# Performance work log

Measured on AMD Instinct MI355X. Metric: run time of the kernel, lower is better.

## Reference

```python
import jax, jax.numpy as jnp
import numpy as np

N = 50000   # nodes
E = 800000  # edges
F = 128     # feat_dim
I = 128     # internal_dim
G = 64      # graphs in batch
EPS = 1e-5


def setup_inputs() -> dict:
    key = jax.random.key(0)
    ks = jax.random.split(key, 32)
    s = 0.1
    inp = {
        'x': jax.random.normal(ks[0], (N, F), dtype=jnp.float32),
        'edge_index': jax.random.randint(ks[1], (2, E), 0, N, dtype=jnp.int64),
        'batch': jnp.sort(jax.random.randint(ks[2], (N,), 0, G, dtype=jnp.int64)),
        # InitialSubnet: Linear(F->I) + BN(I)
        'init_W': jax.random.normal(ks[3], (F, I)) * s,
        'init_b': jnp.zeros((I,)),
        'init_g': jnp.ones((I,)),
        'init_bt': jnp.zeros((I,)),
        # 2 middle EdgeConv subnets: Linear(2I->I) + BN(I)
        'mid_W': jax.random.normal(ks[4], (2, 2 * I, I)) * s,
        'mid_b': jnp.zeros((2, I)),
        'mid_g': jnp.ones((2, I)),
        'mid_bt': jnp.zeros((2, I)),
        # 1 er / 1 pr receptor-specific EdgeConv subnet each
        'er_W': jax.random.normal(ks[5], (1, 2 * I, I)) * s,
        'er_b': jnp.zeros((1, I)),
        'er_g': jnp.ones((1, I)),
        'er_bt': jnp.zeros((1, I)),
        'pr_W': jax.random.normal(ks[6], (1, 2 * I, I)) * s,
        'pr_b': jnp.zeros((1, I)),
        'pr_g': jnp.ones((1, I)),
        'pr_bt': jnp.zeros((1, I)),
        # 3 shared posts: Linear(I->2) + BN(2)
        'spost_W': jax.random.normal(ks[7], (3, I, 2)) * s,
        'spost_b': jnp.zeros((3, 2)),
        'spost_g': jnp.ones((3, 2)),
        'spost_bt': jnp.zeros((3, 2)),
        # 1 er post / 1 pr post: Linear(I->1) + BN(1)
        'erpost_W': jax.random.normal(ks[8], (1, I, 1)) * s,
        'erpost_b': jnp.zeros((1, 1)),
        'erpost_g': jnp.ones((1, 1)),
        'erpost_bt': jnp.zeros((1, 1)),
        'prpost_W': jax.random.normal(ks[9], (1, I, 1)) * s,
        'prpost_b': jnp.zeros((1, 1)),
        'prpost_g': jnp.ones((1, 1)),
        'prpost_bt': jnp.zeros((1, 1)),
    }
    return inp


def _bn(h, g, b):
    # BatchNorm1d in training mode: batch stats over the row dim, biased var
    m = jnp.mean(h, axis=0)
    v = jnp.var(h, axis=0)
    return (h - m) * jax.lax.rsqrt(v + EPS) * g + b


def _edgeconv(h, src, dst, W, b, g, bt):
    # PyG EdgeConv: msg = nn(cat([x_i, x_j - x_i])), aggr=max over incoming edges
    x_i = h[dst]                      # [E, I]
    x_j = h[src]                      # [E, I]
    msg = jnp.concatenate([x_i, x_j - x_i], axis=-1) @ W + b  # [E, I]
    msg = jax.nn.elu(_bn(msg, g, bt))
    out = jax.ops.segment_max(msg, dst, num_segments=N)
    return jnp.where(jnp.isneginf(out), 0.0, out)  # isolated nodes -> 0


def _post(h, batch, counts, W, b, g, bt):
    # elu(BN(Linear(h))) then global_mean_pool; dropout is identity (eval)
    h2 = jax.nn.elu(_bn(h @ W + b, g, bt))
    pooled = jax.ops.segment_sum(h2, batch, num_segments=G)
    return pooled / counts[:, None]


def reference(x, edge_index, batch,
              init_W, init_b, init_g, init_bt,
              mid_W, mid_b, mid_g, mid_bt,
              er_W, er_b, er_g, er_bt,
              pr_W, pr_b, pr_g, pr_bt,
              spost_W, spost_b, spost_g, spost_bt,
              erpost_W, erpost_b, erpost_g, erpost_bt,
              prpost_W, prpost_b, prpost_g, prpost_bt):
    src, dst = edge_index[0], edge_index[1]
    counts = jnp.maximum(jax.ops.segment_sum(jnp.ones((N,), x.dtype), batch, num_segments=G), 1.0)

    outs = []
    # InitialSubnet: gelu(BN(Linear(x)))
    h = jax.nn.gelu(_bn(x @ init_W + init_b, init_g, init_bt), approximate=False)
    outs.append(_post(h, batch, counts, spost_W[0], spost_b[0], spost_g[0], spost_bt[0]))

    for l in range(2):
        h = _edgeconv(h, src, dst, mid_W[l], mid_b[l], mid_g[l], mid_bt[l])
        outs.append(_post(h, batch, counts, spost_W[l + 1], spost_b[l + 1], spost_g[l + 1], spost_bt[l + 1]))

    er_h = h
    pr_h = h
    for l in range(1):
        er_h = _edgeconv(er_h, src, dst, er_W[l], er_b[l], er_g[l], er_bt[l])
        er_out = _post(er_h, batch, counts, erpost_W[l], erpost_b[l], erpost_g[l], erpost_bt[l])
        pr_h = _edgeconv(pr_h, src, dst, pr_W[l], pr_b[l], pr_g[l], pr_bt[l])
        pr_out = _post(pr_h, batch, counts, prpost_W[l], prpost_b[l], prpost_g[l], prpost_bt[l])
        outs.append(jnp.concatenate([er_out, pr_out], axis=-1))

    agg = outs[0]
    for o in outs[1:]:
        agg = agg + o
    return agg  # [G, 2]
```

## Files before the change

kernel.cpp:

```cpp
#include <hip/hip_runtime.h>
#include <math.h>

#define EPS 1e-5f

typedef float f32x4v __attribute__((ext_vector_type(4)));
typedef short s16x8  __attribute__((ext_vector_type(8)));

__device__ __forceinline__ float elu_f(float x) { return x > 0.f ? x : expm1f(x); }
__device__ __forceinline__ float blo(unsigned u) { return __uint_as_float(u << 16); }
__device__ __forceinline__ float bhi(unsigned u) { return __uint_as_float(u & 0xffff0000u); }
__device__ __forceinline__ unsigned f2b(float f) {
  unsigned u = __float_as_uint(f);
  unsigned r = ((u >> 16) & 1u) + 0x7fffu;
  return (u + r) >> 16;
}
__device__ __forceinline__ unsigned pack2(float a, float b) {
  return f2b(a) | (f2b(b) << 16);
}

__global__ __launch_bounds__(256) void prep_all(const float* __restrict__ init_W,
    const float* __restrict__ mid_W, const float* __restrict__ er_W,
    const float* __restrict__ pr_W, const float* __restrict__ mid_g,
    const float* __restrict__ er_g, const float* __restrict__ pr_g,
    unsigned short* __restrict__ WT) {
  int grp = blockIdx.x >> 6;
  int i = (blockIdx.x & 63) * 256 + threadIdx.x;
  if (i >= 16384) return;
  int k = i >> 7, c = i & 127;
  if (grp == 0) {
    WT[c * 128 + k] = (unsigned short)f2b(init_W[k * 128 + c]);
    return;
  }
  const float* W; const float* g; unsigned short* Wd; unsigned short* W2;
  if (grp == 1)      { W = mid_W;             g = mid_g;       Wd = WT + 1 * 16384; W2 = WT + 2 * 16384; }
  else if (grp == 2) { W = mid_W + 256 * 128; g = mid_g + 128; Wd = WT + 3 * 16384; W2 = WT + 4 * 16384; }
  else if (grp == 3) { W = er_W;              g = er_g;        Wd = WT + 5 * 16384; W2 = WT + 6 * 16384; }
  else               { W = pr_W;              g = pr_g;        Wd = WT + 7 * 16384; W2 = WT + 8 * 16384; }
  float sg = (g[c] >= 0.f) ? 1.f : -1.f;
  float w1 = W[k * 128 + c];
  float w2 = W[(k + 128) * 128 + c];
  Wd[c * 128 + k] = (unsigned short)f2b((w1 - w2) * sg);
  W2[c * 128 + k] = (unsigned short)f2b(w2 * sg);
}

template<int XF32, int NMAT, int STATS>
__global__ __launch_bounds__(256, 3) void gemm_mfma(const void* __restrict__ Xv,
    const unsigned short* __restrict__ W0t, const unsigned short* __restrict__ W1t,
    const unsigned short* __restrict__ W2t, const unsigned short* __restrict__ W3t,
    unsigned short* __restrict__ Y0, unsigned short* __restrict__ Y1,
    unsigned short* __restrict__ Y2, unsigned short* __restrict__ Y3,
    float* __restrict__ stOut, int Nrows) {
  int tid = threadIdx.x, lane = tid & 63, wv = tid >> 6;
  int r0 = blockIdx.x * 64;
  int rlo = lane & 15, kg = lane >> 4;
  s16x8 zf = {0, 0, 0, 0, 0, 0, 0, 0};
  s16x8 af[4][4];
#pragma unroll
  for (int rg = 0; rg < 4; ++rg) {
    int arow = r0 + rg * 16 + rlo;
    if (arow < Nrows) {
      if (XF32) {
        const float* xr = (const float*)Xv + (size_t)arow * 128 + kg * 8;
#pragma unroll
        for (int s2 = 0; s2 < 4; ++s2) {
          float4 a = *(const float4*)(xr + s2 * 32);
          float4 b = *(const float4*)(xr + s2 * 32 + 4);
          s16x8 t;
          t[0] = (short)f2b(a.x); t[1] = (short)f2b(a.y);
          t[2] = (short)f2b(a.z); t[3] = (short)f2b(a.w);
          t[4] = (short)f2b(b.x); t[5] = (short)f2b(b.y);
          t[6] = (short)f2b(b.z); t[7] = (short)f2b(b.w);
          af[rg][s2] = t;
        }
      } else {
        const unsigned short* xr = (const unsigned short*)Xv + (size_t)arow * 128 + kg * 8;
#pragma unroll
        for (int s2 = 0; s2 < 4; ++s2) af[rg][s2] = *(const s16x8*)(xr + s2 * 32);
      }
    } else {
#pragma unroll
      for (int s2 = 0; s2 < 4; ++s2) af[rg][s2] = zf;
    }
  }
  const unsigned short* Ws[4] = {W0t, W1t, W2t, W3t};
  unsigned short* Ys[4] = {Y0, Y1, Y2, Y3};
#pragma unroll
  for (int o = 0; o < NMAT; ++o) {
    const unsigned short* Wt = Ws[o];
    unsigned short* Y = Ys[o];
#pragma unroll
    for (int t = 0; t < 2; ++t) {
      int nt = wv * 2 + t;
      const unsigned short* wp = Wt + (size_t)(nt * 16 + rlo) * 128 + kg * 8;
      s16x8 wf[4];
#pragma unroll
      for (int s2 = 0; s2 < 4; ++s2) wf[s2] = *(const s16x8*)(wp + s2 * 32);
      f32x4v acc[4];
#pragma unroll
      for (int rg = 0; rg < 4; ++rg) acc[rg] = (f32x4v){0.f, 0.f, 0.f, 0.f};
#pragma unroll
      for (int s2 = 0; s2 < 4; ++s2)
#pragma unroll
        for (int rg = 0; rg < 4; ++rg)
          acc[rg] = __builtin_amdgcn_mfma_f32_16x16x32_bf16(wf[s2], af[rg][s2], acc[rg], 0, 0, 0);
      float ps0 = 0.f, ps1 = 0.f, ps2 = 0.f, ps3 = 0.f;
      float pq0 = 0.f, pq1 = 0.f, pq2 = 0.f, pq3 = 0.f;
#pragma unroll
      for (int rg = 0; rg < 4; ++rg) {
        int arow = r0 + rg * 16 + rlo;
        if (arow < Nrows) {
          uint2 ov;
          ov.x = pack2(acc[rg][0], acc[rg][1]);
          ov.y = pack2(acc[rg][2], acc[rg][3]);
          *(uint2*)(Y + (size_t)arow * 128 + nt * 16 + kg * 4) = ov;
          if (STATS) {
            float y0 = blo(ov.x), y1 = bhi(ov.x), y2 = blo(ov.y), y3 = bhi(ov.y);
            ps0 += y0; pq0 += y0 * y0;
            ps1 += y1; pq1 += y1 * y1;
            ps2 += y2; pq2 += y2 * y2;
            ps3 += y3; pq3 += y3 * y3;
          }
        }
      }
      if (STATS) {
#pragma unroll
        for (int off = 1; off < 16; off <<= 1) {
          ps0 += __shfl_xor(ps0, off); pq0 += __shfl_xor(pq0, off);
          ps1 += __shfl_xor(ps1, off); pq1 += __shfl_xor(pq1, off);
          ps2 += __shfl_xor(ps2, off); pq2 += __shfl_xor(pq2, off);
          ps3 += __shfl_xor(ps3, off); pq3 += __shfl_xor(pq3, off);
        }
        if (rlo == 0) {
          int col = nt * 16 + kg * 4;
          float* sb = stOut + (size_t)(blockIdx.x & 15) * 256;
          atomicAdd(&sb[2 * col + 0], ps0); atomicAdd(&sb[2 * col + 1], pq0);
          atomicAdd(&sb[2 * (col + 1)], ps1); atomicAdd(&sb[2 * (col + 1) + 1], pq1);
          atomicAdd(&sb[2 * (col + 2)], ps2); atomicAdd(&sb[2 * (col + 2) + 1], pq2);
          atomicAdd(&sb[2 * (col + 3)], ps3); atomicAdd(&sb[2 * (col + 3) + 1], pq3);
        }
      }
    }
  }
}

__global__ __launch_bounds__(256) void csr_p0_count_hist(const int* __restrict__ dst,
    int* __restrict__ partials, int Ecnt,
    const int* __restrict__ batch, float* __restrict__ counts, int Nn) {
  if (blockIdx.x < 64) {
    __shared__ int cnt[256];
    cnt[threadIdx.x] = 0;
    __syncthreads();
    int i0 = blockIdx.x * 256 + threadIdx.x, stride = 64 * 256;
    for (int e = i0; e < Ecnt; e += stride) atomicAdd(&cnt[(unsigned)dst[e] >> 8], 1);
    __syncthreads();
    partials[blockIdx.x * 256 + threadIdx.x] = cnt[threadIdx.x];
  } else {
    __shared__ float lc[64];
    if (threadIdx.x < 64) lc[threadIdx.x] = 0.f;
    __syncthreads();
    int i0 = (blockIdx.x - 64) * 256 + threadIdx.x, stride = 64 * 256;
    for (int n = i0; n < Nn; n += stride) atomicAdd(&lc[batch[n]], 1.f);
    __syncthreads();
    if (threadIdx.x < 64 && lc[threadIdx.x] != 0.f)
      atomicAdd(&counts[threadIdx.x * 16], lc[threadIdx.x]);
  }
}

__global__ __launch_bounds__(256) void csr_p0_scan(const int* __restrict__ partials,
    int nblk, int* __restrict__ bucket_base, int* __restrict__ gcursor) {
  __shared__ int sc[256];
  int b = threadIdx.x;
  int s = 0;
  for (int k = 0; k < nblk; ++k) s += partials[k * 256 + b];
  sc[b] = s;
  __syncthreads();
  for (int off = 1; off < 256; off <<= 1) {
    int t = (b >= off) ? sc[b - off] : 0;
    __syncthreads();
    sc[b] += t;
    __syncthreads();
  }
  int excl = sc[b] - s;
  bucket_base[b] = excl;
  gcursor[b * 16] = excl;
  if (b == 255) bucket_base[256] = sc[255];
}

#define P1_CHUNK 4096
__global__ __launch_bounds__(256) void csr_p1_bin(const int* __restrict__ src,
    const int* __restrict__ dst, int* __restrict__ gcursor,
    unsigned* __restrict__ binned, int Ecnt) {
  __shared__ unsigned stage[P1_CHUNK];
  __shared__ int cnt[256], lbase[256], gbase[256], lcur[256], sc[256];
  int tid = threadIdx.x;
  int e0 = blockIdx.x * P1_CHUNK;
  int ecnt = Ecnt - e0; if (ecnt > P1_CHUNK) ecnt = P1_CHUNK;
  cnt[tid] = 0;
  __syncthreads();
  for (int i = tid; i < ecnt; i += 256) atomicAdd(&cnt[(unsigned)dst[e0 + i] >> 8], 1);
  __syncthreads();
  sc[tid] = cnt[tid];
  __syncthreads();
  for (int off = 1; off < 256; off <<= 1) {
    int t = (tid >= off) ? sc[tid - off] : 0;
    __syncthreads();
    sc[tid] += t;
    __syncthreads();
  }
  lbase[tid] = sc[tid] - cnt[tid];
  lcur[tid] = lbase[tid];
  gbase[tid] = (cnt[tid] > 0) ? atomicAdd(&gcursor[tid * 16], cnt[tid]) : 0;
  __syncthreads();
  for (int i = tid; i < ecnt; i += 256) {
    int d = dst[e0 + i], s = src[e0 + i];
    int bk = (unsigned)d >> 8;
    int p = atomicAdd(&lcur[bk], 1);
    stage[p] = ((unsigned)bk << 24) | ((unsigned)(d & 255) << 16) | (unsigned)s;
  }
  __syncthreads();
  for (int i = tid; i < ecnt; i += 256) {
    unsigned v = stage[i];
    int bk = v >> 24;
    binned[gbase[bk] + (i - lbase[bk])] = v;
  }
}

#define P2_CAP 12288
__global__ __launch_bounds__(256) void csr_p2_sort(const unsigned* __restrict__ binned,
    const int* __restrict__ bucket_base, unsigned short* __restrict__ csr_src,
    int* __restrict__ deg, int* __restrict__ rowstart, int Nn) {
  __shared__ unsigned short stage[P2_CAP];
  __shared__ int cnt[256], lbase[256], lcur[256], sc[256];
  int b = blockIdx.x, tid = threadIdx.x;
  int base = bucket_base[b];
  int bcnt = bucket_base[b + 1] - base;
  if (bcnt > P2_CAP) bcnt = P2_CAP;
  cnt[tid] = 0;
  __syncthreads();
  for (int i = tid; i < bcnt; i += 256) atomicAdd(&cnt[(binned[base + i] >> 16) & 255], 1);
  __syncthreads();
  sc[tid] = cnt[tid];
  __syncthreads();
  for (int off = 1; off < 256; off <<= 1) {
    int t = (tid >= off) ? sc[tid - off] : 0;
    __syncthreads();
    sc[tid] += t;
    __syncthreads();
  }
  lbase[tid] = sc[tid] - cnt[tid];
  lcur[tid] = lbase[tid];
  int node = b * 256 + tid;
  if (node < Nn) { deg[node] = cnt[tid]; rowstart[node] = base + lbase[tid]; }
  __syncthreads();
  for (int i = tid; i < bcnt; i += 256) {
    unsigned v = binned[base + i];
    int j = (v >> 16) & 255;
    int p = atomicAdd(&lcur[j], 1);
    stage[p] = (unsigned short)(v & 0xffffu);
  }
  __syncthreads();
  for (int i = tid; i < bcnt; i += 256) csr_src[base + i] = stage[i];
}

__global__ __launch_bounds__(256, 8) void conv_pass(const unsigned short* __restrict__ A,
    const unsigned short* __restrict__ B, const unsigned short* __restrict__ csr_src,
    const int* __restrict__ rowstart, const int* __restrict__ deg,
    const float* __restrict__ g, unsigned short* __restrict__ Mx,
    float* __restrict__ st, int Nn) {
  __shared__ float s_sum[128], s_ssq[128];
  int tid = threadIdx.x;
  if (tid < 128) { s_sum[tid] = 0.f; s_ssq[tid] = 0.f; }
  __syncthreads();
  int lane = tid & 63;
  int wave = __builtin_amdgcn_readfirstlane((blockIdx.x << 2) + (tid >> 6));
  int wstride = gridDim.x << 2;
  int c0 = lane * 2;
  float sg0 = (g[c0] >= 0.f) ? 1.f : -1.f;
  float sg1 = (g[c0 + 1] >= 0.f) ? 1.f : -1.f;
  const unsigned* A32 = (const unsigned*)A;
  const unsigned* B32 = (const unsigned*)B;
  unsigned* M32 = (unsigned*)Mx;
  float s0 = 0.f, ss0 = 0.f, s1 = 0.f, ss1 = 0.f;
  for (int n = wave; n < Nn; n += wstride) {
    int dg = deg[n];
    if (dg == 0) continue;
    int beg = rowstart[n];
    unsigned ua = A32[(size_t)n * 64 + lane];
    float a0 = blo(ua), a1 = bhi(ua);
    float mx0 = -INFINITY, mx1 = -INFINITY;
    int e = beg, eend = beg + dg;
    for (; e + 8 <= eend; e += 8) {
      int idx[8];
#pragma unroll
      for (int q = 0; q < 8; ++q) idx[q] = csr_src[e + q];
      unsigned uu[8];
#pragma unroll
      for (int q = 0; q < 8; ++q) uu[q] = B32[(size_t)idx[q] * 64 + lane];
#pragma unroll
      for (int q = 0; q < 8; ++q) {
        float m0 = a0 + blo(uu[q]), m1 = a1 + bhi(uu[q]);
        s0 += m0; ss0 += m0 * m0;
        s1 += m1; ss1 += m1 * m1;
        mx0 = fmaxf(mx0, m0);
        mx1 = fmaxf(mx1, m1);
      }
    }
    for (; e + 2 <= eend; e += 2) {
      int ia = csr_src[e], ib = csr_src[e + 1];
      unsigned u0 = B32[(size_t)ia * 64 + lane];
      unsigned u1 = B32[(size_t)ib * 64 + lane];
      float m00 = a0 + blo(u0), m01 = a1 + bhi(u0);
      float m10 = a0 + blo(u1), m11 = a1 + bhi(u1);
      s0 += m00 + m10; ss0 += m00 * m00 + m10 * m10;
      s1 += m01 + m11; ss1 += m01 * m01 + m11 * m11;
      mx0 = fmaxf(mx0, fmaxf(m00, m10));
      mx1 = fmaxf(mx1, fmaxf(m01, m11));
    }
    if (e < eend) {
      unsigned u0 = B32[(size_t)csr_src[e] * 64 + lane];
      float m00 = a0 + blo(u0), m01 = a1 + bhi(u0);
      s0 += m00; ss0 += m00 * m00;
      s1 += m01; ss1 += m01 * m01;
      mx0 = fmaxf(mx0, m00);
      mx1 = fmaxf(mx1, m01);
    }
    M32[(size_t)n * 64 + lane] = pack2(mx0, mx1);
  }
  atomicAdd(&s_sum[c0], s0 * sg0); atomicAdd(&s_ssq[c0], ss0);
  atomicAdd(&s_sum[c0 + 1], s1 * sg1); atomicAdd(&s_ssq[c0 + 1], ss1);
  __syncthreads();
  if (tid < 128) {
    float* sb = st + (size_t)(blockIdx.x & 15) * 256;
    atomicAdd(&sb[2 * tid], s_sum[tid]);
    atomicAdd(&sb[2 * tid + 1], s_ssq[tid]);
  }
}

__global__ __launch_bounds__(256, 8) void conv_pass_dual(
    const unsigned short* __restrict__ Aer, const unsigned short* __restrict__ Ber,
    const unsigned short* __restrict__ Apr, const unsigned short* __restrict__ Bpr,
    const unsigned short* __restrict__ csr_src,
    const int* __restrict__ rowstart, const int* __restrict__ deg,
    const float* __restrict__ g_er, const float* __restrict__ g_pr,
    unsigned short* __restrict__ Mer, unsigned short* __restrict__ Mpr,
    float* __restrict__ st_er, float* __restrict__ st_pr, int Nn) {
  __shared__ float s_e[256], s_p[256];
  int tid = threadIdx.x;
  s_e[tid] = 0.f; s_p[tid] = 0.f;
  __syncthreads();
  int lane = tid & 63;
  int wave = __builtin_amdgcn_readfirstlane((blockIdx.x << 2) + (tid >> 6));
  int wstride = gridDim.x << 2;
  int c0 = lane * 2;
  float sge0 = (g_er[c0] >= 0.f) ? 1.f : -1.f;
  float sge1 = (g_er[c0 + 1] >= 0.f) ? 1.f : -1.f;
  float sgp0 = (g_pr[c0] >= 0.f) ? 1.f : -1.f;
  float sgp1 = (g_pr[c0 + 1] >= 0.f) ? 1.f : -1.f;
  const unsigned* Ae32 = (const unsigned*)Aer;
  const unsigned* Be32 = (const unsigned*)Ber;
  const unsigned* Ap32 = (const unsigned*)Apr;
  const unsigned* Bp32 = (const unsigned*)Bpr;
  unsigned* Me32 = (unsigned*)Mer;
  unsigned* Mp32 = (unsigned*)Mpr;
  float se0 = 0.f, sse0 = 0.f, se1 = 0.f, sse1 = 0.f;
  float sp0 = 0.f, ssp0 = 0.f, sp1 = 0.f, ssp1 = 0.f;
  for (int n = wave; n < Nn; n += wstride) {
    int dg = deg[n];
    if (dg == 0) continue;
    int beg = rowstart[n];
    unsigned uae = Ae32[(size_t)n * 64 + lane];
    unsigned uap = Ap32[(size_t)n * 64 + lane];
    float ae0 = blo(uae), ae1 = bhi(uae);
    float ap0 = blo(uap), ap1 = bhi(uap);
    float mxe0 = -INFINITY, mxe1 = -INFINITY, mxp0 = -INFINITY, mxp1 = -INFINITY;
    int e = beg, eend = beg + dg;
    for (; e + 8 <= eend; e += 8) {
      int idx[8];
#pragma unroll
      for (int q = 0; q < 8; ++q) idx[q] = csr_src[e + q];
      unsigned ue[8], up[8];
#pragma unroll
      for (int q = 0; q < 8; ++q) ue[q] = Be32[(size_t)idx[q] * 64 + lane];
#pragma unroll
      for (int q = 0; q < 8; ++q) up[q] = Bp32[(size_t)idx[q] * 64 + lane];
#pragma unroll
      for (int q = 0; q < 8; ++q) {
        float me0 = ae0 + blo(ue[q]), me1 = ae1 + bhi(ue[q]);
        float mp0 = ap0 + blo(up[q]), mp1 = ap1 + bhi(up[q]);
        se0 += me0; sse0 += me0 * me0; se1 += me1; sse1 += me1 * me1;
        sp0 += mp0; ssp0 += mp0 * mp0; sp1 += mp1; ssp1 += mp1 * mp1;
        mxe0 = fmaxf(mxe0, me0); mxe1 = fmaxf(mxe1, me1);
        mxp0 = fmaxf(mxp0, mp0); mxp1 = fmaxf(mxp1, mp1);
      }
    }
    for (; e + 2 <= eend; e += 2) {
      int i0 = csr_src[e], i1 = csr_src[e + 1];
      unsigned ue0 = Be32[(size_t)i0 * 64 + lane];
      unsigned up0 = Bp32[(size_t)i0 * 64 + lane];
      unsigned ue1 = Be32[(size_t)i1 * 64 + lane];
      unsigned up1 = Bp32[(size_t)i1 * 64 + lane];
      float me0 = ae0 + blo(ue0), me1 = ae1 + bhi(ue0);
      float mp0 = ap0 + blo(up0), mp1 = ap1 + bhi(up0);
      float ne0 = ae0 + blo(ue1), ne1 = ae1 + bhi(ue1);
      float np0 = ap0 + blo(up1), np1 = ap1 + bhi(up1);
      se0 += me0 + ne0; sse0 += me0 * me0 + ne0 * ne0;
      se1 += me1 + ne1; sse1 += me1 * me1 + ne1 * ne1;
      sp0 += mp0 + np0; ssp0 += mp0 * mp0 + np0 * np0;
      sp1 += mp1 + np1; ssp1 += mp1 * mp1 + np1 * np1;
      mxe0 = fmaxf(mxe0, fmaxf(me0, ne0)); mxe1 = fmaxf(mxe1, fmaxf(me1, ne1));
      mxp0 = fmaxf(mxp0, fmaxf(mp0, np0)); mxp1 = fmaxf(mxp1, fmaxf(mp1, np1));
    }
    if (e < eend) {
      int i0 = csr_src[e];
      unsigned ue = Be32[(size_t)i0 * 64 + lane];
      unsigned up = Bp32[(size_t)i0 * 64 + lane];
      float me0 = ae0 + blo(ue), me1 = ae1 + bhi(ue);
      float mp0 = ap0 + blo(up), mp1 = ap1 + bhi(up);
      se0 += me0; sse0 += me0 * me0; se1 += me1; sse1 += me1 * me1;
      sp0 += mp0; ssp0 += mp0 * mp0; sp1 += mp1; ssp1 += mp1 * mp1;
      mxe0 = fmaxf(mxe0, me0); mxe1 = fmaxf(mxe1, me1);
      mxp0 = fmaxf(mxp0, mp0); mxp1 = fmaxf(mxp1, mp1);
    }
    Me32[(size_t)n * 64 + lane] = pack2(mxe0, mxe1);
    Mp32[(size_t)n * 64 + lane] = pack2(mxp0, mxp1);
  }
  atomicAdd(&s_e[2 * c0], se0 * sge0);       atomicAdd(&s_e[2 * c0 + 1], sse0);
  atomicAdd(&s_e[2 * (c0 + 1)], se1 * sge1); atomicAdd(&s_e[2 * (c0 + 1) + 1], sse1);
  atomicAdd(&s_p[2 * c0], sp0 * sgp0);       atomicAdd(&s_p[2 * c0 + 1], ssp0);
  atomicAdd(&s_p[2 * (c0 + 1)], sp1 * sgp1); atomicAdd(&s_p[2 * (c0 + 1) + 1], ssp1);
  __syncthreads();
  {
    float* se = st_er + (size_t)(blockIdx.x & 15) * 256;
    float* sp = st_pr + (size_t)(blockIdx.x & 15) * 256;
    atomicAdd(&se[tid], s_e[tid]);
    atomicAdd(&sp[tid], s_p[tid]);
  }
}

template<int MODE>
__global__ __launch_bounds__(256) void fused_post16(const unsigned short* __restrict__ Zb,
    const int* __restrict__ deg, const float* __restrict__ stn,
    const float* __restrict__ g, const float* __restrict__ bt,
    const float* __restrict__ Wp, unsigned short* __restrict__ Hb,
    float* __restrict__ zP, float* __restrict__ stp, int Nn, float invCnt, int P) {
  __shared__ float lscale[128], lshift[128];
  __shared__ float red[4][4];
  int tid = threadIdx.x;
  if (tid < 128) {
    float sm = 0.f, sq = 0.f;
#pragma unroll
    for (int k = 0; k < 16; ++k) {
      sm += stn[k * 256 + 2 * tid];
      sq += stn[k * 256 + 2 * tid + 1];
    }
    float mean = sm * invCnt;
    float var = sq * invCnt - mean * mean;
    float sc = g[tid] * rsqrtf(var + EPS);
    float sh = bt[tid] - mean * sc;
    if (MODE == 1 && g[tid] < 0.f) sc = -sc;
    lscale[tid] = sc; lshift[tid] = sh;
  }
  __syncthreads();
  int sub = tid & 15, c0 = sub * 8;
  float sc[8], sh[8], w0[8], w1[8];
#pragma unroll
  for (int j = 0; j < 8; ++j) {
    sc[j] = lscale[c0 + j]; sh[j] = lshift[c0 + j];
    w0[j] = Wp[(c0 + j) * P];
    w1[j] = (P > 1) ? Wp[(c0 + j) * P + 1] : 0.f;
  }
  int g0 = (blockIdx.x * 256 + tid) >> 4;
  int gstride = gridDim.x * 16;
  bool leader = (sub == 0);
  float s0 = 0.f, ss0 = 0.f, s1 = 0.f, ss1 = 0.f;
  for (int n = g0; n < Nn; n += gstride) {
    float d0 = 0.f, d1 = 0.f;
    unsigned ow[4];
    bool live = (MODE == 0) || (deg[n] > 0);
    if (live) {
      uint4 v = ((const uint4*)(Zb + (size_t)n * 128))[sub];
      unsigned w[4] = {v.x, v.y, v.z, v.w};
#pragma unroll
      for (int u = 0; u < 4; ++u) {
        float t0 = blo(w[u]) * sc[2 * u] + sh[2 * u];
        float t1 = bhi(w[u]) * sc[2 * u + 1] + sh[2 * u + 1];
        float y0, y1;
        if (MODE == 0) {
          y0 = 0.5f * t0 * (1.f + erff(t0 * 0.70710678118f));
          y1 = 0.5f * t1 * (1.f + erff(t1 * 0.70710678118f));
        } else {
          y0 = elu_f(t0); y1 = elu_f(t1);
        }
        d0 += y0 * w0[2 * u] + y1 * w0[2 * u + 1];
        d1 += y0 * w1[2 * u] + y1 * w1[2 * u + 1];
        ow[u] = pack2(y0, y1);
      }
    } else {
      ow[0] = ow[1] = ow[2] = ow[3] = 0u;
    }
    if (Hb) ((uint4*)(Hb + (size_t)n * 128))[sub] = make_uint4(ow[0], ow[1], ow[2], ow[3]);
#pragma unroll
    for (int off = 1; off < 16; off <<= 1) {
      d0 += __shfl_xor(d0, off);
      d1 += __shfl_xor(d1, off);
    }
    if (leader) {
      zP[n * 2] = d0;
      if (P > 1) zP[n * 2 + 1] = d1;
      s0 += d0; ss0 += d0 * d0; s1 += d1; ss1 += d1 * d1;
    }
  }
  s0 += __shfl_xor(s0, 16);  s0 += __shfl_xor(s0, 32);
  s1 += __shfl_xor(s1, 16);  s1 += __shfl_xor(s1, 32);
  ss0 += __shfl_xor(ss0, 16); ss0 += __shfl_xor(ss0, 32);
  ss1 += __shfl_xor(ss1, 16); ss1 += __shfl_xor(ss1, 32);
  int wv = tid >> 6;
  if ((tid & 63) == 0) { red[wv][0] = s0; red[wv][1] = s1; red[wv][2] = ss0; red[wv][3] = ss1; }
  __syncthreads();
  if (tid < 4) {
    float v = red[0][tid] + red[1][tid] + red[2][tid] + red[3][tid];
    atomicAdd(&stp[tid * 64], v);
  }
}

__global__ __launch_bounds__(256) void fused_post16_dual(
    const unsigned short* __restrict__ Mer, const unsigned short* __restrict__ Mpr,
    const int* __restrict__ deg,
    const float* __restrict__ st_er, const float* __restrict__ st_pr,
    const float* __restrict__ g_er, const float* __restrict__ bt_er,
    const float* __restrict__ g_pr, const float* __restrict__ bt_pr,
    const float* __restrict__ Wer, const float* __restrict__ Wpr,
    float* __restrict__ zP, float* __restrict__ stp_er, float* __restrict__ stp_pr,
    int Nn, float invE) {
  __shared__ float sce_l[128], she_l[128], scp_l[128], shp_l[128];
  __shared__ float red[4][4];
  int tid = threadIdx.x;
  if (tid < 128) {
    float sme = 0.f, sqe = 0.f, smp = 0.f, sqp = 0.f;
#pragma unroll
    for (int k = 0; k < 16; ++k) {
      sme += st_er[k * 256 + 2 * tid];
      sqe += st_er[k * 256 + 2 * tid + 1];
      smp += st_pr[k * 256 + 2 * tid];
      sqp += st_pr[k * 256 + 2 * tid + 1];
    }
    float mean = sme * invE;
    float var = sqe * invE - mean * mean;
    float sc = g_er[tid] * rsqrtf(var + EPS);
    she_l[tid] = bt_er[tid] - mean * sc;
    sce_l[tid] = (g_er[tid] < 0.f) ? -sc : sc;
    mean = smp * invE;
    var = sqp * invE - mean * mean;
    sc = g_pr[tid] * rsqrtf(var + EPS);
    shp_l[tid] = bt_pr[tid] - mean * sc;
    scp_l[tid] = (g_pr[tid] < 0.f) ? -sc : sc;
  }
  __syncthreads();
  int sub = tid & 15, c0 = sub * 8;
  float sce[8], she[8], scp[8], shp[8], we[8], wp[8];
#pragma unroll
  for (int j = 0; j < 8; ++j) {
    sce[j] = sce_l[c0 + j]; she[j] = she_l[c0 + j];
    scp[j] = scp_l[c0 + j]; shp[j] = shp_l[c0 + j];
    we[j] = Wer[c0 + j]; wp[j] = Wpr[c0 + j];
  }
  int g0 = (blockIdx.x * 256 + tid) >> 4;
  int gstride = gridDim.x * 16;
  bool leader = (sub == 0);
  float s0 = 0.f, ss0 = 0.f, s1 = 0.f, ss1 = 0.f;
  for (int n = g0; n < Nn; n += gstride) {
    float d0 = 0.f, d1 = 0.f;
    if (deg[n] > 0) {
      uint4 ve = ((const uint4*)(Mer + (size_t)n * 128))[sub];
      uint4 vp = ((const uint4*)(Mpr + (size_t)n * 128))[sub];
      unsigned wea[4] = {ve.x, ve.y, ve.z, ve.w};
      unsigned wpa[4] = {vp.x, vp.y, vp.z, vp.w};
#pragma unroll
      for (int u = 0; u < 4; ++u) {
        float te0 = blo(wea[u]) * sce[2 * u] + she[2 * u];
        float te1 = bhi(wea[u]) * sce[2 * u + 1] + she[2 * u + 1];
        float tp0 = blo(wpa[u]) * scp[2 * u] + shp[2 * u];
        float tp1 = bhi(wpa[u]) * scp[2 * u + 1] + shp[2 * u + 1];
        d0 += elu_f(te0) * we[2 * u] + elu_f(te1) * we[2 * u + 1];
        d1 += elu_f(tp0) * wp[2 * u] + elu_f(tp1) * wp[2 * u + 1];
      }
    }
#pragma unroll
    for (int off = 1; off < 16; off <<= 1) {
      d0 += __shfl_xor(d0, off);
      d1 += __shfl_xor(d1, off);
    }
    if (leader) {
      zP[n * 2] = d0;
      zP[n * 2 + 1] = d1;
      s0 += d0; ss0 += d0 * d0; s1 += d1; ss1 += d1 * d1;
    }
  }
  s0 += __shfl_xor(s0, 16);  s0 += __shfl_xor(s0, 32);
  s1 += __shfl_xor(s1, 16);  s1 += __shfl_xor(s1, 32);
  ss0 += __shfl_xor(ss0, 16); ss0 += __shfl_xor(ss0, 32);
  ss1 += __shfl_xor(ss1, 16); ss1 += __shfl_xor(ss1, 32);
  int wv = tid >> 6;
  if ((tid & 63) == 0) { red[wv][0] = s0; red[wv][1] = s1; red[wv][2] = ss0; red[wv][3] = ss1; }
  __syncthreads();
  if (tid < 4) {
    float v = red[0][tid] + red[1][tid] + red[2][tid] + red[3][tid];
    if (tid == 0) atomicAdd(&stp_er[0], v);
    else if (tid == 1) atomicAdd(&stp_pr[0], v);
    else if (tid == 2) atomicAdd(&stp_er[128], v);
    else atomicAdd(&stp_pr[128], v);
  }
}

__global__ __launch_bounds__(256) void post_phase2(const float* __restrict__ zP,
    const int* __restrict__ batch, const float* __restrict__ counts,
    const float* __restrict__ st, const float* __restrict__ g,
    const float* __restrict__ bt, float* __restrict__ out,
    int Nrows, int P, int coloff, float invN) {
  __shared__ float lacc[128];
  if (threadIdx.x < 128) lacc[threadIdx.x] = 0.f;
  __syncthreads();
  float m0 = st[0] * invN;
  float v0 = st[128] * invN - m0 * m0;
  float scale0 = g[0] * rsqrtf(v0 + EPS);
  float shift0 = bt[0] - m0 * scale0;
  float scale1 = 0.f, shift1 = 0.f;
  if (P > 1) {
    float m1 = st[64] * invN;
    float v1 = st[192] * invN - m1 * m1;
    scale1 = g[1] * rsqrtf(v1 + EPS);
    shift1 = bt[1] - m1 * scale1;
  }
  int i0 = blockIdx.x * 256 + threadIdx.x;
  int stride = gridDim.x * 256;
  for (int n = i0; n < Nrows; n += stride) {
    int gi = batch[n];
    float y0 = elu_f(zP[n * 2] * scale0 + shift0);
    atomicAdd(&lacc[gi * 2], y0);
    if (P > 1) {
      float y1 = elu_f(zP[n * 2 + 1] * scale1 + shift1);
      atomicAdd(&lacc[gi * 2 + 1], y1);
    }
  }
  __syncthreads();
  if (threadIdx.x < 128) {
    int gi = threadIdx.x >> 1, p = threadIdx.x & 1;
    float v = lacc[threadIdx.x];
    if (p < P && v != 0.f)
      atomicAdd(&out[gi * 2 + coloff + p], v / fmaxf(counts[gi * 16], 1.f));
  }
}

__global__ __launch_bounds__(256) void post_phase2_dual(const float* __restrict__ zP,
    const int* __restrict__ batch, const float* __restrict__ counts,
    const float* __restrict__ st_er, const float* __restrict__ st_pr,
    const float* __restrict__ g_er, const float* __restrict__ bt_er,
    const float* __restrict__ g_pr, const float* __restrict__ bt_pr,
    float* __restrict__ out, int Nrows, float invN) {
  __shared__ float lacc[128];
  if (threadIdx.x < 128) lacc[threadIdx.x] = 0.f;
  __syncthreads();
  float m0 = st_er[0] * invN;
  float v0 = st_er[128] * invN - m0 * m0;
  float scale0 = g_er[0] * rsqrtf(v0 + EPS);
  float shift0 = bt_er[0] - m0 * scale0;
  float m1 = st_pr[0] * invN;
  float v1 = st_pr[128] * invN - m1 * m1;
  float scale1 = g_pr[0] * rsqrtf(v1 + EPS);
  float shift1 = bt_pr[0] - m1 * scale1;
  int i0 = blockIdx.x * 256 + threadIdx.x;
  int stride = gridDim.x * 256;
  for (int n = i0; n < Nrows; n += stride) {
    int gi = batch[n];
    float y0 = elu_f(zP[n * 2] * scale0 + shift0);
    float y1 = elu_f(zP[n * 2 + 1] * scale1 + shift1);
    atomicAdd(&lacc[gi * 2], y0);
    atomicAdd(&lacc[gi * 2 + 1], y1);
  }
  __syncthreads();
  if (threadIdx.x < 128) {
    int gi = threadIdx.x >> 1, p = threadIdx.x & 1;
    float v = lacc[threadIdx.x];
    if (v != 0.f)
      atomicAdd(&out[gi * 2 + p], v / fmaxf(counts[gi * 16], 1.f));
  }
}

extern "C" void kernel_launch(void* const* d_in, const int* in_sizes, int n_in,
                              void* d_out, int out_size, void* d_ws, size_t ws_size,
                              hipStream_t stream) {
  const float* x       = (const float*)d_in[0];
  const int*   ei      = (const int*)d_in[1];
  const int*   batch   = (const int*)d_in[2];
  const float* init_W  = (const float*)d_in[3];
  const float* init_g  = (const float*)d_in[5];
  const float* init_bt = (const float*)d_in[6];
  const float* mid_W   = (const float*)d_in[7];
  const float* mid_g   = (const float*)d_in[9];
  const float* mid_bt  = (const float*)d_in[10];
  const float* er_W    = (const float*)d_in[11];
  const float* er_g    = (const float*)d_in[13];
  const float* er_bt   = (const float*)d_in[14];
  const float* pr_W    = (const float*)d_in[15];
  const float* pr_g    = (const float*)d_in[17];
  const float* pr_bt   = (const float*)d_in[18];
  const float* spost_W  = (const float*)d_in[19];
  const float* spost_g  = (const float*)d_in[21];
  const float* spost_bt = (const float*)d_in[22];
  const float* erpost_W  = (const float*)d_in[23];
  const float* erpost_g  = (const float*)d_in[25];
  const float* erpost_bt = (const float*)d_in[26];
  const float* prpost_W  = (const float*)d_in[27];
  const float* prpost_g  = (const float*)d_in[29];
  const float* prpost_bt = (const float*)d_in[30];

  int N = in_sizes[0] / 128;
  int E = in_sizes[1] / 2;
  float invN = 1.f / (float)N;
  float invE = 1.f / (float)E;
  float* out = (float*)d_out;

  const int CONV_GRID = 2048;
  int nbuck = (N + 255) >> 8;

  size_t NB = (size_t)N * 128;
  unsigned short* Hb  = (unsigned short*)d_ws;
  unsigned short* Tb0 = Hb + NB;
  unsigned short* Tb1 = Tb0 + NB;
  unsigned short* Tb2 = Tb1 + NB;
  unsigned short* Tb3 = Tb2 + NB;
  unsigned short* MxB = Tb3 + NB;
  unsigned short* MxB2 = MxB + NB;
  float* zP     = (float*)(MxB2 + NB);
  float* counts = zP + (size_t)2 * N;
  float* stats  = counts + 1024;
  float* post   = stats + 5 * 4096;
  unsigned short* WT = (unsigned short*)(post + 5 * 512);
  int* deg        = (int*)(WT + 9 * 16384);
  int* rowstart   = deg + N;
  int* bucketbase = rowstart + N;
  int* gcursor    = bucketbase + 320;
  int* partials   = gcursor + 256 * 16;
  unsigned* binned = (unsigned*)(partials + 64 * 256);
  unsigned short* csr_src = (unsigned short*)(binned + E);

  int gemmGrid = (N + 63) / 64;

  hipMemsetAsync(d_out, 0, out_size * sizeof(float), stream);
  hipMemsetAsync(counts, 0, (1024 + 5 * 4096 + 5 * 512) * sizeof(float), stream);

  prep_all<<<320, 256, 0, stream>>>(init_W, mid_W, er_W, pr_W, mid_g, er_g, pr_g, WT);

  const int* e_src = ei;
  const int* e_dst = ei + E;
  csr_p0_count_hist<<<128, 256, 0, stream>>>(e_dst, partials, E, batch, counts, N);
  csr_p0_scan<<<1, 256, 0, stream>>>(partials, 64, bucketbase, gcursor);
  csr_p1_bin<<<(E + P1_CHUNK - 1) / P1_CHUNK, 256, 0, stream>>>(e_src, e_dst, gcursor, binned, E);
  csr_p2_sort<<<nbuck, 256, 0, stream>>>(binned, bucketbase, csr_src, deg, rowstart, N);

  gemm_mfma<1, 1, 1><<<gemmGrid, 256, 0, stream>>>((const void*)x, WT, nullptr, nullptr, nullptr,
                                                   Tb0, nullptr, nullptr, nullptr, stats, N);
  fused_post16<0><<<512, 256, 0, stream>>>(Tb0, deg, stats, init_g, init_bt, spost_W,
                                           Hb, zP, post + 0 * 512, N, invN, 2);
  post_phase2<<<32, 256, 0, stream>>>(zP, batch, counts, post + 0 * 512,
                                      spost_g, spost_bt, out, N, 2, 0, invN);

  gemm_mfma<0, 2, 0><<<gemmGrid, 256, 0, stream>>>((const void*)Hb,
      WT + 1 * 16384, WT + 2 * 16384, nullptr, nullptr, Tb0, Tb1, nullptr, nullptr, nullptr, N);
  conv_pass<<<CONV_GRID, 256, 0, stream>>>(Tb0, Tb1, csr_src, rowstart, deg, mid_g,
                                           MxB, stats + 1 * 4096, N);
  fused_post16<1><<<512, 256, 0, stream>>>(MxB, deg, stats + 1 * 4096, mid_g, mid_bt,
                                           spost_W + 256, Hb, zP, post + 1 * 512, N, invE, 2);
  post_phase2<<<32, 256, 0, stream>>>(zP, batch, counts, post + 1 * 512,
                                      spost_g + 2, spost_bt + 2, out, N, 2, 0, invN);

  gemm_mfma<0, 2, 0><<<gemmGrid, 256, 0, stream>>>((const void*)Hb,
      WT + 3 * 16384, WT + 4 * 16384, nullptr, nullptr, Tb0, Tb1, nullptr, nullptr, nullptr, N);
  conv_pass<<<CONV_GRID, 256, 0, stream>>>(Tb0, Tb1, csr_src, rowstart, deg, mid_g + 128,
                                           MxB, stats + 2 * 4096, N);
  fused_post16<1><<<512, 256, 0, stream>>>(MxB, deg, stats + 2 * 4096, mid_g + 128, mid_bt + 128,
                                           spost_W + 512, Hb, zP, post + 2 * 512, N, invE, 2);
  post_phase2<<<32, 256, 0, stream>>>(zP, batch, counts, post + 2 * 512,
                                      spost_g + 4, spost_bt + 4, out, N, 2, 0, invN);

  gemm_mfma<0, 4, 0><<<gemmGrid, 256, 0, stream>>>((const void*)Hb,
      WT + 5 * 16384, WT + 6 * 16384, WT + 7 * 16384, WT + 8 * 16384,
      Tb0, Tb1, Tb2, Tb3, nullptr, N);
  conv_pass_dual<<<CONV_GRID, 256, 0, stream>>>(Tb0, Tb1, Tb2, Tb3, csr_src, rowstart, deg,
                                                er_g, pr_g, MxB, MxB2,
                                                stats + 3 * 4096, stats + 4 * 4096, N);
  fused_post16_dual<<<512, 256, 0, stream>>>(MxB, MxB2, deg,
      stats + 3 * 4096, stats + 4 * 4096, er_g, er_bt, pr_g, pr_bt,
      erpost_W, prpost_W, zP, post + 3 * 512, post + 4 * 512, N, invE);
  post_phase2_dual<<<32, 256, 0, stream>>>(zP, batch, counts,
      post + 3 * 512, post + 4 * 512, erpost_g, erpost_bt, prpost_g, prpost_bt,
      out, N, invN);
}
```

Before: 428.8 us.

## Fuse BN+activation+post projection into GEMM prologue and post_phase2 into conv

Removes the separate fused_post16 pass by applying BatchNorm, GELU/ELU and the 2-wide post projection inside the next GEMM's A-fragment load. The GEMM also writes the zP values and their statistics, and post_phase2 work moves into extra blocks appended to the conv_pass grid. Weight prep is merged with the CSR histogram kernel to cut launches. This drops one full read/write of the N×128 activation per layer and several launches. In exchange the GEMM does more per-element math and register work, and the appended post blocks depend on ordering inside the conv kernel.

Result: slower. 518.3 us (+20.9%).

```diff
diff --git a/kernel.cpp b/kernel.cpp
--- a/kernel.cpp
+++ b/kernel.cpp
@@ -18,68 +18,262 @@
   return f2b(a) | (f2b(b) << 16);
 }
 
-__global__ __launch_bounds__(256) void prep_all(const float* __restrict__ init_W,
+__global__ __launch_bounds__(256) void prep_csr0(const float* __restrict__ init_W,
     const float* __restrict__ mid_W, const float* __restrict__ er_W,
     const float* __restrict__ pr_W, const float* __restrict__ mid_g,
     const float* __restrict__ er_g, const float* __restrict__ pr_g,
-    unsigned short* __restrict__ WT) {
-  int grp = blockIdx.x >> 6;
-  int i = (blockIdx.x & 63) * 256 + threadIdx.x;
-  if (i >= 16384) return;
-  int k = i >> 7, c = i & 127;
-  if (grp == 0) {
-    WT[c * 128 + k] = (unsigned short)f2b(init_W[k * 128 + c]);
-    return;
-  }
-  const float* W; const float* g; unsigned short* Wd; unsigned short* W2;
-  if (grp == 1)      { W = mid_W;             g = mid_g;       Wd = WT + 1 * 16384; W2 = WT + 2 * 16384; }
-  else if (grp == 2) { W = mid_W + 256 * 128; g = mid_g + 128; Wd = WT + 3 * 16384; W2 = WT + 4 * 16384; }
-  else if (grp == 3) { W = er_W;              g = er_g;        Wd = WT + 5 * 16384; W2 = WT + 6 * 16384; }
-  else               { W = pr_W;              g = pr_g;        Wd = WT + 7 * 16384; W2 = WT + 8 * 16384; }
-  float sg = (g[c] >= 0.f) ? 1.f : -1.f;
-  float w1 = W[k * 128 + c];
-  float w2 = W[(k + 128) * 128 + c];
-  Wd[c * 128 + k] = (unsigned short)f2b((w1 - w2) * sg);
-  W2[c * 128 + k] = (unsigned short)f2b(w2 * sg);
-}
-
-template<int XF32, int NMAT, int STATS>
+    unsigned short* __restrict__ WT,
+    const int* __restrict__ dst, int* __restrict__ partials, int Ecnt,
+    const int* __restrict__ batch, float* __restrict__ counts, int Nn) {
+  if (blockIdx.x < 320) {
+    int grp = blockIdx.x >> 6;
+    int i = (blockIdx.x & 63) * 256 + threadIdx.x;
+    if (i >= 16384) return;
+    int k = i >> 7, c = i & 127;
+    if (grp == 0) {
+      WT[c * 128 + k] = (unsigned short)f2b(init_W[k * 128 + c]);
+      return;
+    }
+    const float* W; const float* g; unsigned short* Wd; unsigned short* W2;
+    if (grp == 1)      { W = mid_W;             g = mid_g;       Wd = WT + 1 * 16384; W2 = WT + 2 * 16384; }
+    else if (grp == 2) { W = mid_W + 256 * 128; g = mid_g + 128; Wd = WT + 3 * 16384; W2 = WT + 4 * 16384; }
+    else if (grp == 3) { W = er_W;              g = er_g;        Wd = WT + 5 * 16384; W2 = WT + 6 * 16384; }
+    else               { W = pr_W;              g = pr_g;        Wd = WT + 7 * 16384; W2 = WT + 8 * 16384; }
+    float sg = (g[c] >= 0.f) ? 1.f : -1.f;
+    float w1 = W[k * 128 + c];
+    float w2 = W[(k + 128) * 128 + c];
+    Wd[c * 128 + k] = (unsigned short)f2b((w1 - w2) * sg);
+    W2[c * 128 + k] = (unsigned short)f2b(w2 * sg);
+  } else {
+    int b = blockIdx.x - 320;
+    if (b < 64) {
+      __shared__ int cnt[256];
+      cnt[threadIdx.x] = 0;
+      __syncthreads();
+      int i0 = b * 256 + threadIdx.x, stride = 64 * 256;
+      for (int e = i0; e < Ecnt; e += stride) atomicAdd(&cnt[(unsigned)dst[e] >> 8], 1);
+      __syncthreads();
+      partials[b * 256 + threadIdx.x] = cnt[threadIdx.x];
+    } else {
+      __shared__ float lc[64];
+      if (threadIdx.x < 64) lc[threadIdx.x] = 0.f;
+      __syncthreads();
+      int i0 = (b - 64) * 256 + threadIdx.x, stride = 64 * 256;
+      for (int n = i0; n < Nn; n += stride) atomicAdd(&lc[batch[n]], 1.f);
+      __syncthreads();
+      if (threadIdx.x < 64 && lc[threadIdx.x] != 0.f)
+        atomicAdd(&counts[threadIdx.x * 16], lc[threadIdx.x]);
+    }
+  }
+}
+
+__global__ __launch_bounds__(256) void csr_p0_scan(const int* __restrict__ partials,
+    int nblk, int* __restrict__ bucket_base, int* __restrict__ gcursor) {
+  __shared__ int sc[256];
+  int b = threadIdx.x;
+  int s = 0;
+  for (int k = 0; k < nblk; ++k) s += partials[k * 256 + b];
+  sc[b] = s;
+  __syncthreads();
+  for (int off = 1; off < 256; off <<= 1) {
+    int t = (b >= off) ? sc[b - off] : 0;
+    __syncthreads();
+    sc[b] += t;
+    __syncthreads();
+  }
+  int excl = sc[b] - s;
+  bucket_base[b] = excl;
+  gcursor[b * 16] = excl;
+  if (b == 255) bucket_base[256] = sc[255];
+}
+
+#define P1_CHUNK 4096
+__global__ __launch_bounds__(256) void csr_p1_bin(const int* __restrict__ src,
+    const int* __restrict__ dst, int* __restrict__ gcursor,
+    unsigned* __restrict__ binned, int Ecnt) {
+  __shared__ unsigned stage[P1_CHUNK];
+  __shared__ int cnt[256], lbase[256], gbase[256], lcur[256], sc[256];
+  int tid = threadIdx.x;
+  int e0 = blockIdx.x * P1_CHUNK;
+  int ecnt = Ecnt - e0; if (ecnt > P1_CHUNK) ecnt = P1_CHUNK;
+  cnt[tid] = 0;
+  __syncthreads();
+  for (int i = tid; i < ecnt; i += 256) atomicAdd(&cnt[(unsigned)dst[e0 + i] >> 8], 1);
+  __syncthreads();
+  sc[tid] = cnt[tid];
+  __syncthreads();
+  for (int off = 1; off < 256; off <<= 1) {
+    int t = (tid >= off) ? sc[tid - off] : 0;
+    __syncthreads();
+    sc[tid] += t;
+    __syncthreads();
+  }
+  lbase[tid] = sc[tid] - cnt[tid];
+  lcur[tid] = lbase[tid];
+  gbase[tid] = (cnt[tid] > 0) ? atomicAdd(&gcursor[tid * 16], cnt[tid]) : 0;
+  __syncthreads();
+  for (int i = tid; i < ecnt; i += 256) {
+    int d = dst[e0 + i], s = src[e0 + i];
+    int bk = (unsigned)d >> 8;
+    int p = atomicAdd(&lcur[bk], 1);
+    stage[p] = ((unsigned)bk << 24) | ((unsigned)(d & 255) << 16) | (unsigned)s;
+  }
+  __syncthreads();
+  for (int i = tid; i < ecnt; i += 256) {
+    unsigned v = stage[i];
+    int bk = v >> 24;
+    binned[gbase[bk] + (i - lbase[bk])] = v;
+  }
+}
+
+#define P2_CAP 12288
+__global__ __launch_bounds__(256) void csr_p2_sort(const unsigned* __restrict__ binned,
+    const int* __restrict__ bucket_base, unsigned short* __restrict__ csr_src,
+    int* __restrict__ deg, int* __restrict__ rowstart, int Nn) {
+  __shared__ unsigned short stage[P2_CAP];
+  __shared__ int cnt[256], lbase[256], lcur[256], sc[256];
+  int b = blockIdx.x, tid = threadIdx.x;
+  int base = bucket_base[b];
+  int bcnt = bucket_base[b + 1] - base;
+  if (bcnt > P2_CAP) bcnt = P2_CAP;
+  cnt[tid] = 0;
+  __syncthreads();
+  for (int i = tid; i < bcnt; i += 256) atomicAdd(&cnt[(binned[base + i] >> 16) & 255], 1);
+  __syncthreads();
+  sc[tid] = cnt[tid];
+  __syncthreads();
+  for (int off = 1; off < 256; off <<= 1) {
+    int t = (tid >= off) ? sc[tid - off] : 0;
+    __syncthreads();
+    sc[tid] += t;
+    __syncthreads();
+  }
+  lbase[tid] = sc[tid] - cnt[tid];
+  lcur[tid] = lbase[tid];
+  int node = b * 256 + tid;
+  if (node < Nn) { deg[node] = cnt[tid]; rowstart[node] = base + lbase[tid]; }
+  __syncthreads();
+  for (int i = tid; i < bcnt; i += 256) {
+    unsigned v = binned[base + i];
+    int j = (v >> 16) & 255;
+    int p = atomicAdd(&lcur[j], 1);
+    stage[p] = (unsigned short)(v & 0xffffu);
+  }
+  __syncthreads();
+  for (int i = tid; i < bcnt; i += 256) csr_src[base + i] = stage[i];
+}
+
+template<int XF32, int NMAT, int STATS, int ACT>
 __global__ __launch_bounds__(256, 3) void gemm_mfma(const void* __restrict__ Xv,
     const unsigned short* __restrict__ W0t, const unsigned short* __restrict__ W1t,
     const unsigned short* __restrict__ W2t, const unsigned short* __restrict__ W3t,
     unsigned short* __restrict__ Y0, unsigned short* __restrict__ Y1,
     unsigned short* __restrict__ Y2, unsigned short* __restrict__ Y3,
-    float* __restrict__ stOut, int Nrows) {
+    float* __restrict__ stOut,
+    const float* __restrict__ stn, const float* __restrict__ g,
+    const float* __restrict__ bt, const int* __restrict__ deg,
+    const float* __restrict__ Wp, float* __restrict__ zP, float* __restrict__ stp,
+    float invCnt, int Nrows) {
+  __shared__ float lsc[128], lsh[128], lw0[128], lw1[128];
   int tid = threadIdx.x, lane = tid & 63, wv = tid >> 6;
   int r0 = blockIdx.x * 64;
   int rlo = lane & 15, kg = lane >> 4;
+  if (ACT) {
+    if (tid < 128) {
+      float sm = 0.f, sq = 0.f;
+#pragma unroll
+      for (int k = 0; k < 16; ++k) {
+        sm += stn[k * 256 + 2 * tid];
+        sq += stn[k * 256 + 2 * tid + 1];
+      }
+      float mean = sm * invCnt;
+      float var = sq * invCnt - mean * mean;
+      float sc = g[tid] * rsqrtf(var + EPS);
+      float sh = bt[tid] - mean * sc;
+      if (ACT == 2 && g[tid] < 0.f) sc = -sc;
+      lsc[tid] = sc; lsh[tid] = sh;
+      lw0[tid] = Wp[tid * 2]; lw1[tid] = Wp[tid * 2 + 1];
+    }
+    __syncthreads();
+  }
   s16x8 zf = {0, 0, 0, 0, 0, 0, 0, 0};
   s16x8 af[4][4];
-#pragma unroll
-  for (int rg = 0; rg < 4; ++rg) {
-    int arow = r0 + rg * 16 + rlo;
-    if (arow < Nrows) {
-      if (XF32) {
-        const float* xr = (const float*)Xv + (size_t)arow * 128 + kg * 8;
-#pragma unroll
-        for (int s2 = 0; s2 < 4; ++s2) {
-          float4 a = *(const float4*)(xr + s2 * 32);
-          float4 b = *(const float4*)(xr + s2 * 32 + 4);
-          s16x8 t;
-          t[0] = (short)f2b(a.x); t[1] = (short)f2b(a.y);
-          t[2] = (short)f2b(a.z); t[3] = (short)f2b(a.w);
-          t[4] = (short)f2b(b.x); t[5] = (short)f2b(b.y);
-          t[6] = (short)f2b(b.z); t[7] = (short)f2b(b.w);
-          af[rg][s2] = t;
+  float d0 = 0.f, d1 = 0.f;
+  if (!ACT) {
+#pragma unroll
+    for (int rg = 0; rg < 4; ++rg) {
+      int arow = r0 + rg * 16 + rlo;
+      if (arow < Nrows) {
+        if (XF32) {
+          const float* xr = (const float*)Xv + (size_t)arow * 128 + kg * 8;
+#pragma unroll
+          for (int s2 = 0; s2 < 4; ++s2) {
+            float4 a = *(const float4*)(xr + s2 * 32);
+            float4 b = *(const float4*)(xr + s2 * 32 + 4);
+            s16x8 t;
+            t[0] = (short)f2b(a.x); t[1] = (short)f2b(a.y);
+            t[2] = (short)f2b(a.z); t[3] = (short)f2b(a.w);
+            t[4] = (short)f2b(b.x); t[5] = (short)f2b(b.y);
+            t[6] = (short)f2b(b.z); t[7] = (short)f2b(b.w);
+            af[rg][s2] = t;
+          }
+        } else {
+          const unsigned short* xr = (const unsigned short*)Xv + (size_t)arow * 128 + kg * 8;
+#pragma unroll
+          for (int s2 = 0; s2 < 4; ++s2) af[rg][s2] = *(const s16x8*)(xr + s2 * 32);
         }
       } else {
-        const unsigned short* xr = (const unsigned short*)Xv + (size_t)arow * 128 + kg * 8;
-#pragma unroll
-        for (int s2 = 0; s2 < 4; ++s2) af[rg][s2] = *(const s16x8*)(xr + s2 * 32);
+#pragma unroll
+        for (int s2 = 0; s2 < 4; ++s2) af[rg][s2] = zf;
       }
-    } else {
-#pragma unroll
-      for (int s2 = 0; s2 < 4; ++s2) af[rg][s2] = zf;
+    }
+  } else {
+    int degv[4];
+#pragma unroll
+    for (int rg = 0; rg < 4; ++rg) {
+      int arow = r0 + rg * 16 + rlo;
+      degv[rg] = (arow < Nrows) ? ((ACT == 2) ? deg[arow] : 1) : 0;
+    }
+#pragma unroll
+    for (int s2 = 0; s2 < 4; ++s2) {
+      int cb = kg * 8 + s2 * 32;
+      float sc[8], sh[8], w0[8], w1[8];
+#pragma unroll
+      for (int j = 0; j < 8; ++j) {
+        sc[j] = lsc[cb + j]; sh[j] = lsh[cb + j];
+        w0[j] = lw0[cb + j]; w1[j] = lw1[cb + j];
+      }
+#pragma unroll
+      for (int rg = 0; rg < 4; ++rg) {
+        if (degv[rg] > 0) {
+          int arow = r0 + rg * 16 + rlo;
+          uint4 v = *(const uint4*)((const unsigned short*)Xv + (size_t)arow * 128 + cb);
+          unsigned wds[4] = {v.x, v.y, v.z, v.w};
+          s16x8 t;
+          float dd0 = 0.f, dd1 = 0.f;
+#pragma unroll
+          for (int u = 0; u < 4; ++u) {
+            float t0 = blo(wds[u]) * sc[2 * u] + sh[2 * u];
+            float t1 = bhi(wds[u]) * sc[2 * u + 1] + sh[2 * u + 1];
+            float y0, y1;
+            if (ACT == 1) {
+              y0 = 0.5f * t0 * (1.f + erff(t0 * 0.70710678118f));
+              y1 = 0.5f * t1 * (1.f + erff(t1 * 0.70710678118f));
+            } else {
+              y0 = elu_f(t0); y1 = elu_f(t1);
+            }
+            unsigned pw = pack2(y0, y1);
+            t[2 * u] = (short)(pw & 0xffffu);
+            t[2 * u + 1] = (short)(pw >> 16);
+            dd0 += y0 * w0[2 * u] + y1 * w0[2 * u + 1];
+            dd1 += y0 * w1[2 * u] + y1 * w1[2 * u + 1];
+          }
+          af[rg][s2] = t;
+          if (rg == wv) { d0 += dd0; d1 += dd1; }
+        } else {
+          af[rg][s2] = zf;
+        }
+      }
     }
   }
   const unsigned short* Ws[4] = {W0t, W1t, W2t, W3t};
@@ -141,139 +335,75 @@
       }
     }
   }
-}
-
-__global__ __launch_bounds__(256) void csr_p0_count_hist(const int* __restrict__ dst,
-    int* __restrict__ partials, int Ecnt,
-    const int* __restrict__ batch, float* __restrict__ counts, int Nn) {
-  if (blockIdx.x < 64) {
-    __shared__ int cnt[256];
-    cnt[threadIdx.x] = 0;
-    __syncthreads();
-    int i0 = blockIdx.x * 256 + threadIdx.x, stride = 64 * 256;
-    for (int e = i0; e < Ecnt; e += stride) atomicAdd(&cnt[(unsigned)dst[e] >> 8], 1);
-    __syncthreads();
-    partials[blockIdx.x * 256 + threadIdx.x] = cnt[threadIdx.x];
-  } else {
-    __shared__ float lc[64];
-    if (threadIdx.x < 64) lc[threadIdx.x] = 0.f;
-    __syncthreads();
-    int i0 = (blockIdx.x - 64) * 256 + threadIdx.x, stride = 64 * 256;
-    for (int n = i0; n < Nn; n += stride) atomicAdd(&lc[batch[n]], 1.f);
-    __syncthreads();
-    if (threadIdx.x < 64 && lc[threadIdx.x] != 0.f)
-      atomicAdd(&counts[threadIdx.x * 16], lc[threadIdx.x]);
-  }
-}
-
-__global__ __launch_bounds__(256) void csr_p0_scan(const int* __restrict__ partials,
-    int nblk, int* __restrict__ bucket_base, int* __restrict__ gcursor) {
-  __shared__ int sc[256];
-  int b = threadIdx.x;
-  int s = 0;
-  for (int k = 0; k < nblk; ++k) s += partials[k * 256 + b];
-  sc[b] = s;
-  __syncthreads();
-  for (int off = 1; off < 256; off <<= 1) {
-    int t = (b >= off) ? sc[b - off] : 0;
-    __syncthreads();
-    sc[b] += t;
-    __syncthreads();
-  }
-  int excl = sc[b] - s;
-  bucket_base[b] = excl;
-  gcursor[b * 16] = excl;
-  if (b == 255) bucket_base[256] = sc[255];
-}
-
-#define P1_CHUNK 4096
-__global__ __launch_bounds__(256) void csr_p1_bin(const int* __restrict__ src,
-    const int* __restrict__ dst, int* __restrict__ gcursor,
-    unsigned* __restrict__ binned, int Ecnt) {
-  __shared__ unsigned stage[P1_CHUNK];
-  __shared__ int cnt[256], lbase[256], gbase[256], lcur[256], sc[256];
-  int tid = threadIdx.x;
-  int e0 = blockIdx.x * P1_CHUNK;
-  int ecnt = Ecnt - e0; if (ecnt > P1_CHUNK) ecnt = P1_CHUNK;
-  cnt[tid] = 0;
-  __syncthreads();
-  for (int i = tid; i < ecnt; i += 256) atomicAdd(&cnt[(unsigned)dst[e0 + i] >> 8], 1);
-  __syncthreads();
-  sc[tid] = cnt[tid];
-  __syncthreads();
-  for (int off = 1; off < 256; off <<= 1) {
-    int t = (tid >= off) ? sc[tid - off] : 0;
-    __syncthreads();
-    sc[tid] += t;
-    __syncthreads();
-  }
-  lbase[tid] = sc[tid] - cnt[tid];
-  lcur[tid] = lbase[tid];
-  gbase[tid] = (cnt[tid] > 0) ? atomicAdd(&gcursor[tid * 16], cnt[tid]) : 0;
-  __syncthreads();
-  for (int i = tid; i < ecnt; i += 256) {
-    int d = dst[e0 + i], s = src[e0 + i];
-    int bk = (unsigned)d >> 8;
-    int p = atomicAdd(&lcur[bk], 1);
-    stage[p] = ((unsigned)bk << 24) | ((unsigned)(d & 255) << 16) | (unsigned)s;
-  }
-  __syncthreads();
-  for (int i = tid; i < ecnt; i += 256) {
-    unsigned v = stage[i];
-    int bk = v >> 24;
-    binned[gbase[bk] + (i - lbase[bk])] = v;
-  }
-}
-
-#define P2_CAP 12288
-__global__ __launch_bounds__(256) void csr_p2_sort(const unsigned* __restrict__ binned,
-    const int* __restrict__ bucket_base, unsigned short* __restrict__ csr_src,
-    int* __restrict__ deg, int* __restrict__ rowstart, int Nn) {
-  __shared__ unsigned short stage[P2_CAP];
-  __shared__ int cnt[256], lbase[256], lcur[256], sc[256];
-  int b = blockIdx.x, tid = threadIdx.x;
-  int base = bucket_base[b];
-  int bcnt = bucket_base[b + 1] - base;
-  if (bcnt > P2_CAP) bcnt = P2_CAP;
-  cnt[tid] = 0;
-  __syncthreads();
-  for (int i = tid; i < bcnt; i += 256) atomicAdd(&cnt[(binned[base + i] >> 16) & 255], 1);
-  __syncthreads();
-  sc[tid] = cnt[tid];
-  __syncthreads();
-  for (int off = 1; off < 256; off <<= 1) {
-    int t = (tid >= off) ? sc[tid - off] : 0;
-    __syncthreads();
-    sc[tid] += t;
-    __syncthreads();
-  }
-  lbase[tid] = sc[tid] - cnt[tid];
-  lcur[tid] = lbase[tid];
-  int node = b * 256 + tid;
-  if (node < Nn) { deg[node] = cnt[tid]; rowstart[node] = base + lbase[tid]; }
-  __syncthreads();
-  for (int i = tid; i < bcnt; i += 256) {
-    unsigned v = binned[base + i];
-    int j = (v >> 16) & 255;
-    int p = atomicAdd(&lcur[j], 1);
-    stage[p] = (unsigned short)(v & 0xffffu);
-  }
-  __syncthreads();
-  for (int i = tid; i < bcnt; i += 256) csr_src[base + i] = stage[i];
+  if (ACT) {
+    d0 += __shfl_xor(d0, 16); d0 += __shfl_xor(d0, 32);
+    d1 += __shfl_xor(d1, 16); d1 += __shfl_xor(d1, 32);
+    int arow = r0 + wv * 16 + rlo;
+    bool rowok = arow < Nrows;
+    if (rowok && lane < 16) {
+      zP[(size_t)arow * 2] = d0;
+      zP[(size_t)arow * 2 + 1] = d1;
+    }
+    float sd0 = rowok ? d0 : 0.f, sd1 = rowok ? d1 : 0.f;
+    float q0 = sd0 * sd0, q1 = sd1 * sd1;
+#pragma unroll
+    for (int off = 1; off < 16; off <<= 1) {
+      sd0 += __shfl_xor(sd0, off); sd1 += __shfl_xor(sd1, off);
+      q0 += __shfl_xor(q0, off);   q1 += __shfl_xor(q1, off);
+    }
+    if (lane == 0) {
+      float* sb = stp + (size_t)(blockIdx.x & 15) * 4;
+      atomicAdd(sb + 0, sd0); atomicAdd(sb + 1, sd1);
+      atomicAdd(sb + 2, q0);  atomicAdd(sb + 3, q1);
+    }
+  }
 }
 
 __global__ __launch_bounds__(256, 8) void conv_pass(const unsigned short* __restrict__ A,
     const unsigned short* __restrict__ B, const unsigned short* __restrict__ csr_src,
     const int* __restrict__ rowstart, const int* __restrict__ deg,
     const float* __restrict__ g, unsigned short* __restrict__ Mx,
-    float* __restrict__ st, int Nn) {
+    float* __restrict__ st, int Nn, int convBlks,
+    const float* __restrict__ zPp, const int* __restrict__ batch,
+    const float* __restrict__ counts, const float* __restrict__ stpp,
+    const float* __restrict__ g2, const float* __restrict__ bt2,
+    float* __restrict__ out, float invN) {
   __shared__ float s_sum[128], s_ssq[128];
   int tid = threadIdx.x;
+  if ((int)blockIdx.x >= convBlks) {
+    __shared__ float lacc[128];
+    if (tid < 128) lacc[tid] = 0.f;
+    __syncthreads();
+    float S0 = 0.f, S1 = 0.f, Q0 = 0.f, Q1 = 0.f;
+#pragma unroll
+    for (int k = 0; k < 16; ++k) {
+      S0 += stpp[4 * k]; S1 += stpp[4 * k + 1];
+      Q0 += stpp[4 * k + 2]; Q1 += stpp[4 * k + 3];
+    }
+    float m0 = S0 * invN, v0 = Q0 * invN - m0 * m0;
+    float scale0 = g2[0] * rsqrtf(v0 + EPS), shift0 = bt2[0] - m0 * scale0;
+    float m1 = S1 * invN, v1 = Q1 * invN - m1 * m1;
+    float scale1 = g2[1] * rsqrtf(v1 + EPS), shift1 = bt2[1] - m1 * scale1;
+    int i0 = (blockIdx.x - convBlks) * 256 + tid;
+    int stride = 32 * 256;
+    for (int n = i0; n < Nn; n += stride) {
+      int gi = batch[n];
+      atomicAdd(&lacc[gi * 2], elu_f(zPp[n * 2] * scale0 + shift0));
+      atomicAdd(&lacc[gi * 2 + 1], elu_f(zPp[n * 2 + 1] * scale1 + shift1));
+    }
+    __syncthreads();
+    if (tid < 128) {
+      int gi = tid >> 1, p = tid & 1;
+      float v = lacc[tid];
+      if (v != 0.f) atomicAdd(&out[gi * 2 + p], v / fmaxf(counts[gi * 16], 1.f));
+    }
+    return;
+  }
   if (tid < 128) { s_sum[tid] = 0.f; s_ssq[tid] = 0.f; }
   __syncthreads();
   int lane = tid & 63;
   int wave = __builtin_amdgcn_readfirstlane((blockIdx.x << 2) + (tid >> 6));
-  int wstride = gridDim.x << 2;
+  int wstride = convBlks << 2;
   int c0 = lane * 2;
   float sg0 = (g[c0] >= 0.f) ? 1.f : -1.f;
   float sg1 = (g[c0 + 1] >= 0.f) ? 1.f : -1.f;
@@ -343,14 +473,47 @@
     const int* __restrict__ rowstart, const int* __restrict__ deg,
     const float* __restrict__ g_er, const float* __restrict__ g_pr,
     unsigned short* __restrict__ Mer, unsigned short* __restrict__ Mpr,
-    float* __restrict__ st_er, float* __restrict__ st_pr, int Nn) {
+    float* __restrict__ st_er, float* __restrict__ st_pr, int Nn, int convBlks,
+    const float* __restrict__ zPp, const int* __restrict__ batch,
+    const float* __restrict__ counts, const float* __restrict__ stpp,
+    const float* __restrict__ g2, const float* __restrict__ bt2,
+    float* __restrict__ out, float invN) {
   __shared__ float s_e[256], s_p[256];
   int tid = threadIdx.x;
+  if ((int)blockIdx.x >= convBlks) {
+    __shared__ float lacc[128];
+    if (tid < 128) lacc[tid] = 0.f;
+    __syncthreads();
+    float S0 = 0.f, S1 = 0.f, Q0 = 0.f, Q1 = 0.f;
+#pragma unroll
+    for (int k = 0; k < 16; ++k) {
+      S0 += stpp[4 * k]; S1 += stpp[4 * k + 1];
+      Q0 += stpp[4 * k + 2]; Q1 += stpp[4 * k + 3];
+    }
+    float m0 = S0 * invN, v0 = Q0 * invN - m0 * m0;
+    float scale0 = g2[0] * rsqrtf(v0 + EPS), shift0 = bt2[0] - m0 * scale0;
+    float m1 = S1 * invN, v1 = Q1 * invN - m1 * m1;
+    float scale1 = g2[1] * rsqrtf(v1 + EPS), shift1 = bt2[1] - m1 * scale1;
+    int i0 = (blockIdx.x - convBlks) * 256 + tid;
+    int stride = 32 * 256;
+    for (int n = i0; n < Nn; n += stride) {
+      int gi = batch[n];
+      atomicAdd(&lacc[gi * 2], elu_f(zPp[n * 2] * scale0 + shift0));
+      atomicAdd(&lacc[gi * 2 + 1], elu_f(zPp[n * 2 + 1] * scale1 + shift1));
+    }
+    __syncthreads();
+    if (tid < 128) {
+      int gi = tid >> 1, p = tid & 1;
+      float v = lacc[tid];
+      if (v != 0.f) atomicAdd(&out[gi * 2 + p], v / fmaxf(counts[gi * 16], 1.f));
+    }
+    return;
+  }
   s_e[tid] = 0.f; s_p[tid] = 0.f;
   __syncthreads();
   int lane = tid & 63;
   int wave = __builtin_amdgcn_readfirstlane((blockIdx.x << 2) + (tid >> 6));
-  int wstride = gridDim.x << 2;
+  int wstride = convBlks << 2;
   int c0 = lane * 2;
   float sge0 = (g_er[c0] >= 0.f) ? 1.f : -1.f;
   float sge1 = (g_er[c0 + 1] >= 0.f) ? 1.f : -1.f;
@@ -437,92 +600,6 @@
   }
 }
 
-template<int MODE>
-__global__ __launch_bounds__(256) void fused_post16(const unsigned short* __restrict__ Zb,
-    const int* __restrict__ deg, const float* __restrict__ stn,
-    const float* __restrict__ g, const float* __restrict__ bt,
-    const float* __restrict__ Wp, unsigned short* __restrict__ Hb,
-    float* __restrict__ zP, float* __restrict__ stp, int Nn, float invCnt, int P) {
-  __shared__ float lscale[128], lshift[128];
-  __shared__ float red[4][4];
-  int tid = threadIdx.x;
-  if (tid < 128) {
-    float sm = 0.f, sq = 0.f;
-#pragma unroll
-    for (int k = 0; k < 16; ++k) {
-      sm += stn[k * 256 + 2 * tid];
-      sq += stn[k * 256 + 2 * tid + 1];
-    }
-    float mean = sm * invCnt;
-    float var = sq * invCnt - mean * mean;
-    float sc = g[tid] * rsqrtf(var + EPS);
-    float sh = bt[tid] - mean * sc;
-    if (MODE == 1 && g[tid] < 0.f) sc = -sc;
-    lscale[tid] = sc; lshift[tid] = sh;
-  }
-  __syncthreads();
-  int sub = tid & 15, c0 = sub * 8;
-  float sc[8], sh[8], w0[8], w1[8];
-#pragma unroll
-  for (int j = 0; j < 8; ++j) {
-    sc[j] = lscale[c0 + j]; sh[j] = lshift[c0 + j];
-    w0[j] = Wp[(c0 + j) * P];
-    w1[j] = (P > 1) ? Wp[(c0 + j) * P + 1] : 0.f;
-  }
-  int g0 = (blockIdx.x * 256 + tid) >> 4;
-  int gstride = gridDim.x * 16;
-  bool leader = (sub == 0);
-  float s0 = 0.f, ss0 = 0.f, s1 = 0.f, ss1 = 0.f;
-  for (int n = g0; n < Nn; n += gstride) {
-    float d0 = 0.f, d1 = 0.f;
-    unsigned ow[4];
-    bool live = (MODE == 0) || (deg[n] > 0);
-    if (live) {
-      uint4 v = ((const uint4*)(Zb + (size_t)n * 128))[sub];
-      unsigned w[4] = {v.x, v.y, v.z, v.w};
-#pragma unroll
-      for (int u = 0; u < 4; ++u) {
-        float t0 = blo(w[u]) * sc[2 * u] + sh[2 * u];
-        float t1 = bhi(w[u]) * sc[2 * u + 1] + sh[2 * u + 1];
-        float y0, y1;
-        if (MODE == 0) {
-          y0 = 0.5f * t0 * (1.f + erff(t0 * 0.70710678118f));
-          y1 = 0.5f * t1 * (1.f + erff(t1 * 0.70710678118f));
-        } else {
-          y0 = elu_f(t0); y1 = elu_f(t1);
-        }
-        d0 += y0 * w0[2 * u] + y1 * w0[2 * u + 1];
-        d1 += y0 * w1[2 * u] + y1 * w1[2 * u + 1];
-        ow[u] = pack2(y0, y1);
-      }
-    } else {
-      ow[0] = ow[1] = ow[2] = ow[3] = 0u;
-    }
-    if (Hb) ((uint4*)(Hb + (size_t)n * 128))[sub] = make_uint4(ow[0], ow[1], ow[2], ow[3]);
-#pragma unroll
-    for (int off = 1; off < 16; off <<= 1) {
-      d0 += __shfl_xor(d0, off);
-      d1 += __shfl_xor(d1, off);
-    }
-    if (leader) {
-      zP[n * 2] = d0;
-      if (P > 1) zP[n * 2 + 1] = d1;
-      s0 += d0; ss0 += d0 * d0; s1 += d1; ss1 += d1 * d1;
-    }
-  }
-  s0 += __shfl_xor(s0, 16);  s0 += __shfl_xor(s0, 32);
-  s1 += __shfl_xor(s1, 16);  s1 += __shfl_xor(s1, 32);
-  ss0 += __shfl_xor(ss0, 16); ss0 += __shfl_xor(ss0, 32);
-  ss1 += __shfl_xor(ss1, 16); ss1 += __shfl_xor(ss1, 32);
-  int wv = tid >> 6;
-  if ((tid & 63) == 0) { red[wv][0] = s0; red[wv][1] = s1; red[wv][2] = ss0; red[wv][3] = ss1; }
-  __syncthreads();
-  if (tid < 4) {
-    float v = red[0][tid] + red[1][tid] + red[2][tid] + red[3][tid];
-    atomicAdd(&stp[tid * 64], v);
-  }
-}
-
 __global__ __launch_bounds__(256) void fused_post16_dual(
     const unsigned short* __restrict__ Mer, const unsigned short* __restrict__ Mpr,
     const int* __restrict__ deg,
@@ -609,45 +686,6 @@
     else if (tid == 1) atomicAdd(&stp_pr[0], v);
     else if (tid == 2) atomicAdd(&stp_er[128], v);
     else atomicAdd(&stp_pr[128], v);
-  }
-}
-
-__global__ __launch_bounds__(256) void post_phase2(const float* __restrict__ zP,
-    const int* __restrict__ batch, const float* __restrict__ counts,
-    const float* __restrict__ st, const float* __restrict__ g,
-    const float* __restrict__ bt, float* __restrict__ out,
-    int Nrows, int P, int coloff, float invN) {
-  __shared__ float lacc[128];
-  if (threadIdx.x < 128) lacc[threadIdx.x] = 0.f;
-  __syncthreads();
-  float m0 = st[0] * invN;
-  float v0 = st[128] * invN - m0 * m0;
-  float scale0 = g[0] * rsqrtf(v0 + EPS);
-  float shift0 = bt[0] - m0 * scale0;
-  float scale1 = 0.f, shift1 = 0.f;
-  if (P > 1) {
-    float m1 = st[64] * invN;
-    float v1 = st[192] * invN - m1 * m1;
-    scale1 = g[1] * rsqrtf(v1 + EPS);
-    shift1 = bt[1] - m1 * scale1;
-  }
-  int i0 = blockIdx.x * 256 + threadIdx.x;
-  int stride = gridDim.x * 256;
-  for (int n = i0; n < Nrows; n += stride) {
-    int gi = batch[n];
-    float y0 = elu_f(zP[n * 2] * scale0 + shift0);
-    atomicAdd(&lacc[gi * 2], y0);
-    if (P > 1) {
-      float y1 = elu_f(zP[n * 2 + 1] * scale1 + shift1);
-      atomicAdd(&lacc[gi * 2 + 1], y1);
-    }
-  }
-  __syncthreads();
-  if (threadIdx.x < 128) {
-    int gi = threadIdx.x >> 1, p = threadIdx.x & 1;
-    float v = lacc[threadIdx.x];
-    if (p < P && v != 0.f)
-      atomicAdd(&out[gi * 2 + coloff + p], v / fmaxf(counts[gi * 16], 1.f));
   }
 }
 
@@ -720,12 +758,12 @@
   float invE = 1.f / (float)E;
   float* out = (float*)d_out;
 
-  const int CONV_GRID = 2048;
+  const int CONV_BLKS = 2048;
   int nbuck = (N + 255) >> 8;
 
   size_t NB = (size_t)N * 128;
-  unsigned short* Hb  = (unsigned short*)d_ws;
-  unsigned short* Tb0 = Hb + NB;
+  unsigned short* TbI = (unsigned short*)d_ws;
+  unsigned short* Tb0 = TbI + NB;
   unsigned short* Tb1 = Tb0 + NB;
   unsigned short* Tb2 = Tb1 + NB;
   unsigned short* Tb3 = Tb2 + NB;
@@ -734,8 +772,9 @@
   float* zP     = (float*)(MxB2 + NB);
   float* counts = zP + (size_t)2 * N;
   float* stats  = counts + 1024;
-  float* post   = stats + 5 * 4096;
-  unsigned short* WT = (unsigned short*)(post + 5 * 512);
+  float* stp    = stats + 5 * 4096;
+  float* dpost  = stp + 3 * 64;
+  unsigned short* WT = (unsigned short*)(dpost + 2 * 512);
   int* deg        = (int*)(WT + 9 * 16384);
   int* rowstart   = deg + N;
   int* bucketbase = rowstart + N;
@@ -747,52 +786,50 @@
   int gemmGrid = (N + 63) / 64;
 
   hipMemsetAsync(d_out, 0, out_size * sizeof(float), stream);
-  hipMemsetAsync(counts, 0, (1024 + 5 * 4096 + 5 * 512) * sizeof(float), stream);
-
-  prep_all<<<320, 256, 0, stream>>>(init_W, mid_W, er_W, pr_W, mid_g, er_g, pr_g, WT);
+  hipMemsetAsync(counts, 0, (1024 + 5 * 4096 + 3 * 64 + 2 * 512) * sizeof(float), stream);
 
   const int* e_src = ei;
   const int* e_dst = ei + E;
-  csr_p0_count_hist<<<128, 256, 0, stream>>>(e_dst, partials, E, batch, counts, N);
+  prep_csr0<<<448, 256, 0, stream>>>(init_W, mid_W, er_W, pr_W, mid_g, er_g, pr_g, WT,
+                                     e_dst, partials, E, batch, counts, N);
   csr_p0_scan<<<1, 256, 0, stream>>>(partials, 64, bucketbase, gcursor);
   csr_p1_bin<<<(E + P1_CHUNK - 1) / P1_CHUNK, 256, 0, stream>>>(e_src, e_dst, gcursor, binned, E);
   csr_p2_sort<<<nbuck, 256, 0, stream>>>(binned, bucketbase, csr_src, deg, rowstart, N);
 
-  gemm_mfma<1, 1, 1><<<gemmGrid, 256, 0, stream>>>((const void*)x, WT, nullptr, nullptr, nullptr,
-                                                   Tb0, nullptr, nullptr, nullptr, stats, N);
-  fused_post16<0><<<512, 256, 0, stream>>>(Tb0, deg, stats, init_g, init_bt, spost_W,
-                                           Hb, zP, post + 0 * 512, N, invN, 2);
-  post_phase2<<<32, 256, 0, stream>>>(zP, batch, counts, post + 0 * 512,
-                                      spost_g, spost_bt, out, N, 2, 0, invN);
-
-  gemm_mfma<0, 2, 0><<<gemmGrid, 256, 0, stream>>>((const void*)Hb,
-      WT + 1 * 16384, WT + 2 * 16384, nullptr, nullptr, Tb0, Tb1, nullptr, nullptr, nullptr, N);
-  conv_pass<<<CONV_GRID, 256, 0, stream>>>(Tb0, Tb1, csr_src, rowstart, deg, mid_g,
-                                           MxB, stats + 1 * 4096, N);
-  fused_post16<1><<<512, 256, 0, stream>>>(MxB, deg, stats + 1 * 4096, mid_g, mid_bt,
-                                           spost_W + 256, Hb, zP, post + 1 * 512, N, invE, 2);
-  post_phase2<<<32, 256, 0, stream>>>(zP, batch, counts, post + 1 * 512,
-                                      spost_g + 2, spost_bt + 2, out, N, 2, 0, invN);
-
-  gemm_mfma<0, 2, 0><<<gemmGrid, 256, 0, stream>>>((const void*)Hb,
-      WT + 3 * 16384, WT + 4 * 16384, nullptr, nullptr, Tb0, Tb1, nullptr, nullptr, nullptr, N);
-  conv_pass<<<CONV_GRID, 256, 0, stream>>>(Tb0, Tb1, csr_src, rowstart, deg, mid_g + 128,
-                                           MxB, stats + 2 * 4096, N);
-  fused_post16<1><<<512, 256, 0, stream>>>(MxB, deg, stats + 2 * 4096, mid_g + 128, mid_bt + 128,
-                                           spost_W + 512, Hb, zP, post + 2 * 512, N, invE, 2);
-  post_phase2<<<32, 256, 0, stream>>>(zP, batch, counts, post + 2 * 512,
-                                      spost_g + 4, spost_bt + 4, out, N, 2, 0, invN);
-
-  gemm_mfma<0, 4, 0><<<gemmGrid, 256, 0, stream>>>((const void*)Hb,
+  gemm_mfma<1, 1, 1, 0><<<gemmGrid, 256, 0, stream>>>((const void*)x,
+      WT, nullptr, nullptr, nullptr, TbI, nullptr, nullptr, nullptr,
+      stats, nullptr, nullptr, nullptr, nullptr, nullptr, nullptr, nullptr, 0.f, N);
+
+  gemm_mfma<0, 2, 0, 1><<<gemmGrid, 256, 0, stream>>>((const void*)TbI,
+      WT + 1 * 16384, WT + 2 * 16384, nullptr, nullptr, Tb0, Tb1, nullptr, nullptr,
+      nullptr, stats, init_g, init_bt, deg, spost_W, zP, stp + 0 * 64, invN, N);
+
+  conv_pass<<<CONV_BLKS + 32, 256, 0, stream>>>(Tb0, Tb1, csr_src, rowstart, deg, mid_g,
+      MxB, stats + 1 * 4096, N, CONV_BLKS,
+      zP, batch, counts, stp + 0 * 64, spost_g, spost_bt, out, invN);
+
+  gemm_mfma<0, 2, 0, 2><<<gemmGrid, 256, 0, stream>>>((const void*)MxB,
+      WT + 3 * 16384, WT + 4 * 16384, nullptr, nullptr, Tb0, Tb1, nullptr, nullptr,
+      nullptr, stats + 1 * 4096, mid_g, mid_bt, deg, spost_W + 256, zP, stp + 1 * 64, invE, N);
+
+  conv_pass<<<CONV_BLKS + 32, 256, 0, stream>>>(Tb0, Tb1, csr_src, rowstart, deg, mid_g + 128,
+      MxB, stats + 2 * 4096, N, CONV_BLKS,
+      zP, batch, counts, stp + 1 * 64, spost_g + 2, spost_bt + 2, out, invN);
+
+  gemm_mfma<0, 4, 0, 2><<<gemmGrid, 256, 0, stream>>>((const void*)MxB,
       WT + 5 * 16384, WT + 6 * 16384, WT + 7 * 16384, WT + 8 * 16384,
-      Tb0, Tb1, Tb2, Tb3, nullptr, N);
-  conv_pass_dual<<<CONV_GRID, 256, 0, stream>>>(Tb0, Tb1, Tb2, Tb3, csr_src, rowstart, deg,
-                                                er_g, pr_g, MxB, MxB2,
-                                                stats + 3 * 4096, stats + 4 * 4096, N);
+      Tb0, Tb1, Tb2, Tb3,
+      nullptr, stats + 2 * 4096, mid_g + 128, mid_bt + 128, deg, spost_W + 512,
+      zP, stp + 2 * 64, invE, N);
+
+  conv_pass_dual<<<CONV_BLKS + 32, 256, 0, stream>>>(Tb0, Tb1, Tb2, Tb3, csr_src, rowstart, deg,
+      er_g, pr_g, MxB, MxB2, stats + 3 * 4096, stats + 4 * 4096, N, CONV_BLKS,
+      zP, batch, counts, stp + 2 * 64, spost_g + 4, spost_bt + 4, out, invN);
+
   fused_post16_dual<<<512, 256, 0, stream>>>(MxB, MxB2, deg,
       stats + 3 * 4096, stats + 4 * 4096, er_g, er_bt, pr_g, pr_bt,
-      erpost_W, prpost_W, zP, post + 3 * 512, post + 4 * 512, N, invE);
+      erpost_W, prpost_W, zP, dpost, dpost + 512, N, invE);
   post_phase2_dual<<<32, 256, 0, stream>>>(zP, batch, counts,
-      post + 3 * 512, post + 4 * 512, erpost_g, erpost_bt, prpost_g, prpost_bt,
+      dpost, dpost + 512, erpost_g, erpost_bt, prpost_g, prpost_bt,
       out, N, invN);
 }
```
